# Kernel tuning notes

Hardware: AMD Instinct MI355X
Metric: run time of the kernel (lower is better)

## Reference

```python
import jax, jax.numpy as jnp
import numpy as np

MARGIN = 1.0
EPS = 1e-6  # F.pairwise_distance adds eps to the elementwise diff


def setup_inputs() -> dict:
    key = jax.random.key(0)
    k1, k2, k3 = jax.random.split(key, 3)
    N, D = 8192, 64
    anchor_embeddings = jax.random.normal(k1, (N, D), dtype=jnp.float32)
    positive_embeddings = jax.random.normal(k2, (N, D), dtype=jnp.float32)
    labels = jax.random.randint(k3, (N,), 0, 2, dtype=jnp.int64)
    return {
        "anchor_embeddings": anchor_embeddings,
        "positive_embeddings": positive_embeddings,
        "labels": labels,
    }


def _pairwise_dist(a, p):
    # dist[i, j] = ||(a_i + eps) - p_j||_2, matching F.pairwise_distance's
    # norm(x1 - x2 + eps). Computed via the Gram trick to avoid an [N,N,D]
    # intermediate.
    a = a + EPS
    a2 = jnp.sum(a * a, axis=-1)                      # [N]
    p2 = jnp.sum(p * p, axis=-1)                      # [N]
    sq = a2[:, None] + p2[None, :] - 2.0 * (a @ p.T)  # [N, N]
    return jnp.sqrt(jnp.maximum(sq, 1e-12))


def reference(anchor_embeddings, positive_embeddings, labels):
    N = anchor_embeddings.shape[0]
    dist = _pairwise_dist(anchor_embeddings, positive_embeddings)  # [N, N]
    pos_dist = jnp.diagonal(dist)                                  # [N], d(a_i, p_i)
    hinge = jax.nn.relu(pos_dist[:, None] - dist + MARGIN)         # [N, N]
    # pair (i, j) contributes iff labels[i] == 1 and i != j
    row_mask = (labels == 1)[:, None]
    offdiag = ~jnp.eye(N, dtype=bool)
    mask = (row_mask & offdiag).astype(hinge.dtype)
    count = jnp.sum(mask)
    total = jnp.sum(hinge * mask)
    return jnp.where(count > 0, total / jnp.maximum(count, 1.0), 0.0)
```

## Files before the change

### kernel.cpp

```cpp
#include <hip/hip_runtime.h>
#include <hip/hip_bf16.h>

#define NROWS 8192
#define DDIM 64
#define MARGIN_F 1.0f
#define EPS_F 1e-6f


typedef __attribute__((ext_vector_type(8))) short bf16x8;
typedef __attribute__((ext_vector_type(4))) float f32x4;

static __device__ __forceinline__ unsigned short f2bf(float x) {
    __hip_bfloat16 h = __float2bfloat16(x);
    return *reinterpret_cast<unsigned short*>(&h);
}
static __device__ __forceinline__ float bf2f(unsigned short u) {
    return __uint_as_float(((unsigned)u) << 16);
}

__global__ __launch_bounds__(256) void
prep_compact_kernel(const float* __restrict__ A, const float* __restrict__ P,
                    const int* __restrict__ labels,
                    unsigned short* __restrict__ Abf, unsigned short* __restrict__ Pbf,
                    float* __restrict__ a2g, float* __restrict__ pdg,
                    float* __restrict__ p2g, float* __restrict__ hdg,
                    int* __restrict__ sel, int* __restrict__ cnt) {
    __shared__ int lab[256 * 33];
    __shared__ int scan[256];
    int t = threadIdx.x;

    if (blockIdx.x < 512) {
        int gid = blockIdx.x * 256 + t;
        int row = gid >> 4;
        int c4  = (gid & 15) * 4;
        float4 a = *(const float4*)&A[row * DDIM + c4];
        float4 p = *(const float4*)&P[row * DDIM + c4];
        a.x += EPS_F; a.y += EPS_F; a.z += EPS_F; a.w += EPS_F;
        ushort4 ab, pb;
        ab.x = f2bf(a.x); ab.y = f2bf(a.y); ab.z = f2bf(a.z); ab.w = f2bf(a.w);
        pb.x = f2bf(p.x); pb.y = f2bf(p.y); pb.z = f2bf(p.z); pb.w = f2bf(p.w);
        *(ushort4*)&Abf[row * DDIM + c4] = ab;
        *(ushort4*)&Pbf[row * DDIM + c4] = pb;
        float va2 = a.x*a.x + a.y*a.y + a.z*a.z + a.w*a.w;
        float vp2 = p.x*p.x + p.y*p.y + p.z*p.z + p.w*p.w;
        float vap = a.x*p.x + a.y*p.y + a.z*p.z + a.w*p.w;
        float vdd = bf2f(ab.x)*bf2f(pb.x) + bf2f(ab.y)*bf2f(pb.y)
                  + bf2f(ab.z)*bf2f(pb.z) + bf2f(ab.w)*bf2f(pb.w);
        #pragma unroll
        for (int off = 8; off; off >>= 1) {
            va2 += __shfl_xor(va2, off);
            vp2 += __shfl_xor(vp2, off);
            vap += __shfl_xor(vap, off);
            vdd += __shfl_xor(vdd, off);
        }
        if ((t & 15) == 0) {
            a2g[row] = va2;
            p2g[row] = vp2;
            float pd = sqrtf(fmaxf(va2 + vp2 - 2.0f * vap, 1e-12f)) + MARGIN_F;
            pdg[row] = pd;
            float sqd = fmaxf(va2 + vp2 - 2.0f * vdd, 1e-12f);
            hdg[row] = fmaxf(pd - __builtin_amdgcn_sqrtf(sqd), 0.0f);
        }
    } else {
        #pragma unroll
        for (int i = 0; i < 32; ++i) {
            int j = i * 256 + t;
            lab[(j >> 5) * 33 + (j & 31)] = labels[j];
        }
        __syncthreads();
        int lc = 0;
        #pragma unroll
        for (int i = 0; i < 32; ++i) lc += (lab[t * 33 + i] == 1) ? 1 : 0;
        scan[t] = lc;
        __syncthreads();
        for (int off = 1; off < 256; off <<= 1) {
            int v = (t >= off) ? scan[t - off] : 0;
            __syncthreads();
            if (t >= off) scan[t] += v;
            __syncthreads();
        }
        int o = scan[t] - lc;
        for (int i = 0; i < 32; ++i) {
            if (lab[t * 33 + i] == 1) sel[o++] = t * 32 + i;
        }
        if (t == 255) *cnt = scan[255];
    }
}

__global__ __launch_bounds__(256) void
main_kernel(const unsigned short* __restrict__ Abf, const unsigned short* __restrict__ Pbf,
            const float* __restrict__ a2g, const float* __restrict__ pdg,
            const float* __restrict__ p2g, const int* __restrict__ sel,
            const int* __restrict__ cnt, float* __restrict__ partial) {
    __shared__ float sA2[128], sPd[128], sP2[128];
    __shared__ int   sGi[128];
    __shared__ float wsum[4];

    int M = *cnt;
    int row0 = blockIdx.y << 7;
    int col0 = blockIdx.x << 7;
    int bid  = (blockIdx.y << 6) + blockIdx.x;
    int t = threadIdx.x;
    if (row0 >= M) { if (t == 0) partial[bid] = 0.0f; return; }

    int wid  = t >> 6;
    int lane = t & 63;
    int wm   = (wid >> 1) << 6;
    int wn   = (wid & 1) << 6;
    int lm   = lane & 15;
    int quad = lane >> 4;

    bf16x8 bg[2][4];
    #pragma unroll
    for (int b = 0; b < 4; ++b) {
        const unsigned short* pb = Pbf + (size_t)(col0 + wn + b * 16 + lm) * DDIM + quad * 8;
        bg[0][b] = *(const bf16x8*)pb;
        bg[1][b] = *(const bf16x8*)(pb + 32);
    }

    if (t < 128) {
        int gi = sel[min(row0 + t, M - 1)];
        sGi[t] = gi;
        sA2[t] = a2g[gi];
        sPd[t] = pdg[gi];
        sP2[t] = p2g[col0 + t];
    }
    __syncthreads();

    bf16x8 af[2][4];
    #pragma unroll
    for (int a = 0; a < 4; ++a) {
        const unsigned short* pa = Abf + (size_t)sGi[wm + a * 16 + lm] * DDIM + quad * 8;
        af[0][a] = *(const bf16x8*)pa;
        af[1][a] = *(const bf16x8*)(pa + 32);
    }

    f32x4 acc[4][4] = {};
    #pragma unroll
    for (int s = 0; s < 2; ++s)
        #pragma unroll
        for (int a = 0; a < 4; ++a)
            #pragma unroll
            for (int b = 0; b < 4; ++b)
                acc[a][b] = __builtin_amdgcn_mfma_f32_16x16x32_bf16(af[s][a], bg[s][b], acc[a][b], 0, 0, 0);

    float spv[4];
    #pragma unroll
    for (int b = 0; b < 4; ++b) spv[b] = sP2[wn + b * 16 + lm];

    float bsum = 0.0f;
    #pragma unroll
    for (int a = 0; a < 4; ++a) {
        #pragma unroll
        for (int r = 0; r < 4; ++r) {
            int il = wm + a * 16 + quad * 4 + r;
            float rm  = ((row0 + il) < M) ? 1.0f : 0.0f;
            float ra2 = sA2[il];
            float rpd = sPd[il];
            #pragma unroll
            for (int b = 0; b < 4; ++b) {
                float sq = fmaf(-2.0f, acc[a][b][r], ra2 + spv[b]);
                float h  = rpd - __builtin_amdgcn_sqrtf(sq);
                bsum = fmaf(fmaxf(h, 0.0f), rm, bsum);
            }
        }
    }

    #pragma unroll
    for (int off = 32; off; off >>= 1) bsum += __shfl_xor(bsum, off);
    if (lane == 0) wsum[wid] = bsum;
    __syncthreads();
    if (t == 0) partial[bid] = wsum[0] + wsum[1] + wsum[2] + wsum[3];
}

__global__ __launch_bounds__(256) void
finalize_kernel(const int* __restrict__ cnt, const float* __restrict__ partial,
                const float* __restrict__ hdg, const int* __restrict__ sel,
                float* __restrict__ out) {
    __shared__ float wsum[4];
    int t = threadIdx.x;
    const float4* p4 = (const float4*)partial;
    float s = 0.0f;
    #pragma unroll
    for (int i = 0; i < 4; ++i) {
        float4 v = p4[i * 256 + t];
        s += v.x + v.y + v.z + v.w;
    }
    int M = *cnt;
    for (int idx = t; idx < M; idx += 256) s -= hdg[sel[idx]];
    #pragma unroll
    for (int off = 32; off; off >>= 1) s += __shfl_xor(s, off);
    if ((t & 63) == 0) wsum[t >> 6] = s;
    __syncthreads();
    if (t == 0) {
        float tot = wsum[0] + wsum[1] + wsum[2] + wsum[3];
        float c = (float)M * (float)(NROWS - 1);
        out[0] = (M > 0) ? tot / c : 0.0f;
    }
}

extern "C" void kernel_launch(void* const* d_in, const int* in_sizes, int n_in,
                              void* d_out, int out_size, void* d_ws, size_t ws_size,
                              hipStream_t stream) {
    const float* A      = (const float*)d_in[0];
    const float* P      = (const float*)d_in[1];
    const int*   labels = (const int*)d_in[2];
    float* out = (float*)d_out;

    char* ws = (char*)d_ws;
    unsigned short* Abf = (unsigned short*)(ws);
    unsigned short* Pbf = (unsigned short*)(ws + (1 << 20));
    float* a2g     = (float*)(ws + (2 << 20));
    float* pdg     = (float*)(ws + (2 << 20) + 32768);
    float* p2g     = (float*)(ws + (2 << 20) + 65536);
    int*   sel     = (int*)(ws + (2 << 20) + 98304);
    int*   cnt     = (int*)(ws + (2 << 20) + 131072);
    float* partial = (float*)(ws + (2 << 20) + 135168);
    float* hdg     = (float*)(ws + (2 << 20) + 151552);

    prep_compact_kernel<<<dim3(513), dim3(256), 0, stream>>>(A, P, labels, Abf, Pbf,
                                                             a2g, pdg, p2g, hdg, sel, cnt);

    dim3 grid(NROWS / 128, NROWS / 128);
    main_kernel<<<grid, dim3(256), 0, stream>>>(Abf, Pbf, a2g, pdg, p2g, sel, cnt, partial);

    finalize_kernel<<<1, dim3(256), 0, stream>>>(cnt, partial, hdg, sel, out);
}
```

Measured before the change: 89.96 us.

## Fuse finalize into main kernel via last-block reduction and widen column tiles

Removes the separate finalize launch: each main-kernel block writes its partial sum, bumps an atomic counter, and the last block to finish performs the final reduction and the diagonal correction. Each block now covers four 128-column tiles in a loop, so the grid shrinks from 64x64 to 16x64 and the A fragments and row constants are loaded once per block instead of once per tile. Invalid padded rows are masked by setting their positive distance to a large negative value, which drops the per-element multiply mask. The trade-offs are fewer blocks in flight and an atomic plus threadfence on every block.

```diff
diff --git a/kernel.cpp b/kernel.cpp
--- a/kernel.cpp
+++ b/kernel.cpp
@@ -5,6 +5,7 @@
 #define DDIM 64
 #define MARGIN_F 1.0f
 #define EPS_F 1e-6f
+#define NEG_BIG -1.0e30f
 
 
 typedef __attribute__((ext_vector_type(8))) short bf16x8;
@@ -24,7 +25,8 @@
                     unsigned short* __restrict__ Abf, unsigned short* __restrict__ Pbf,
                     float* __restrict__ a2g, float* __restrict__ pdg,
                     float* __restrict__ p2g, float* __restrict__ hdg,
-                    int* __restrict__ sel, int* __restrict__ cnt) {
+                    int* __restrict__ sel, int* __restrict__ cnt,
+                    unsigned int* __restrict__ done) {
     __shared__ int lab[256 * 33];
     __shared__ int scan[256];
     int t = threadIdx.x;
@@ -62,6 +64,7 @@
             hdg[row] = fmaxf(pd - __builtin_amdgcn_sqrtf(sqd), 0.0f);
         }
     } else {
+        if (t == 0) *done = 0u;
         #pragma unroll
         for (int i = 0; i < 32; ++i) {
             int j = i * 256 + t;
@@ -90,112 +93,125 @@
 __global__ __launch_bounds__(256) void
 main_kernel(const unsigned short* __restrict__ Abf, const unsigned short* __restrict__ Pbf,
             const float* __restrict__ a2g, const float* __restrict__ pdg,
-            const float* __restrict__ p2g, const int* __restrict__ sel,
-            const int* __restrict__ cnt, float* __restrict__ partial) {
-    __shared__ float sA2[128], sPd[128], sP2[128];
+            const float* __restrict__ p2g, const float* __restrict__ hdg,
+            const int* __restrict__ sel, const int* __restrict__ cnt,
+            float* __restrict__ partial, unsigned int* __restrict__ done,
+            float* __restrict__ out) {
+    __shared__ float sA2[128], sPd[128];
     __shared__ int   sGi[128];
     __shared__ float wsum[4];
+    __shared__ int   lastFlag;
 
     int M = *cnt;
+    int t = threadIdx.x;
     int row0 = blockIdx.y << 7;
-    int col0 = blockIdx.x << 7;
-    int bid  = (blockIdx.y << 6) + blockIdx.x;
-    int t = threadIdx.x;
-    if (row0 >= M) { if (t == 0) partial[bid] = 0.0f; return; }
+    int bid  = (blockIdx.y << 4) + blockIdx.x;
 
     int wid  = t >> 6;
     int lane = t & 63;
-    int wm   = (wid >> 1) << 6;
-    int wn   = (wid & 1) << 6;
-    int lm   = lane & 15;
-    int quad = lane >> 4;
-
-    bf16x8 bg[2][4];
-    #pragma unroll
-    for (int b = 0; b < 4; ++b) {
-        const unsigned short* pb = Pbf + (size_t)(col0 + wn + b * 16 + lm) * DDIM + quad * 8;
-        bg[0][b] = *(const bf16x8*)pb;
-        bg[1][b] = *(const bf16x8*)(pb + 32);
-    }
-
-    if (t < 128) {
-        int gi = sel[min(row0 + t, M - 1)];
-        sGi[t] = gi;
-        sA2[t] = a2g[gi];
-        sPd[t] = pdg[gi];
-        sP2[t] = p2g[col0 + t];
+
+    if (row0 < M) {
+        if (t < 128) {
+            int ri = row0 + t;
+            int gi = sel[min(ri, M - 1)];
+            sGi[t] = gi;
+            sA2[t] = a2g[gi];
+            sPd[t] = (ri < M) ? pdg[gi] : NEG_BIG;
+        }
+        __syncthreads();
+
+        int wm   = (wid >> 1) << 6;
+        int wn   = (wid & 1) << 6;
+        int lm   = lane & 15;
+        int quad = lane >> 4;
+
+        bf16x8 af0[4], af1[4];
+        #pragma unroll
+        for (int a = 0; a < 4; ++a) {
+            const unsigned short* pa = Abf + (size_t)sGi[wm + a * 16 + lm] * DDIM + quad * 8;
+            af0[a] = *(const bf16x8*)pa;
+            af1[a] = *(const bf16x8*)(pa + 32);
+        }
+        float ra2s[16], rpds[16];
+        #pragma unroll
+        for (int a = 0; a < 4; ++a)
+            #pragma unroll
+            for (int r = 0; r < 4; ++r) {
+                int il = wm + a * 16 + quad * 4 + r;
+                ra2s[a * 4 + r] = sA2[il];
+                rpds[a * 4 + r] = sPd[il];
+            }
+
+        float bsum = 0.0f;
+        #pragma unroll 1
+        for (int i = 0; i < 4; ++i) {
+            int col0 = (blockIdx.x << 9) + (i << 7);
+            bf16x8 bg0[4], bg1[4];
+            float spv[4];
+            #pragma unroll
+            for (int b = 0; b < 4; ++b) {
+                int cj = col0 + wn + b * 16 + lm;
+                const unsigned short* pb = Pbf + (size_t)cj * DDIM + quad * 8;
+                bg0[b] = *(const bf16x8*)pb;
+                bg1[b] = *(const bf16x8*)(pb + 32);
+                spv[b] = p2g[cj];
+            }
+            f32x4 acc[4][4] = {};
+            #pragma unroll
+            for (int a = 0; a < 4; ++a)
+                #pragma unroll
+                for (int b = 0; b < 4; ++b)
+                    acc[a][b] = __builtin_amdgcn_mfma_f32_16x16x32_bf16(af0[a], bg0[b], acc[a][b], 0, 0, 0);
+            #pragma unroll
+            for (int a = 0; a < 4; ++a)
+                #pragma unroll
+                for (int b = 0; b < 4; ++b)
+                    acc[a][b] = __builtin_amdgcn_mfma_f32_16x16x32_bf16(af1[a], bg1[b], acc[a][b], 0, 0, 0);
+
+            #pragma unroll
+            for (int a = 0; a < 4; ++a)
+                #pragma unroll
+                for (int r = 0; r < 4; ++r) {
+                    float ra2 = ra2s[a * 4 + r];
+                    float rpd = rpds[a * 4 + r];
+                    #pragma unroll
+                    for (int b = 0; b < 4; ++b) {
+                        float sq = fmaf(-2.0f, acc[a][b][r], ra2 + spv[b]);
+                        float h  = rpd - __builtin_amdgcn_sqrtf(sq);
+                        bsum += fmaxf(h, 0.0f);
+                    }
+                }
+        }
+
+        #pragma unroll
+        for (int off = 32; off; off >>= 1) bsum += __shfl_xor(bsum, off);
+        if (lane == 0) wsum[wid] = bsum;
+        __syncthreads();
+    }
+
+    if (t == 0) {
+        float s = (row0 < M) ? (wsum[0] + wsum[1] + wsum[2] + wsum[3]) : 0.0f;
+        partial[bid] = s;
+        __threadfence();
+        unsigned v = atomicAdd(done, 1u);
+        lastFlag = (v == 1023u);
     }
     __syncthreads();
-
-    bf16x8 af[2][4];
-    #pragma unroll
-    for (int a = 0; a < 4; ++a) {
-        const unsigned short* pa = Abf + (size_t)sGi[wm + a * 16 + lm] * DDIM + quad * 8;
-        af[0][a] = *(const bf16x8*)pa;
-        af[1][a] = *(const bf16x8*)(pa + 32);
-    }
-
-    f32x4 acc[4][4] = {};
-    #pragma unroll
-    for (int s = 0; s < 2; ++s)
-        #pragma unroll
-        for (int a = 0; a < 4; ++a)
-            #pragma unroll
-            for (int b = 0; b < 4; ++b)
-                acc[a][b] = __builtin_amdgcn_mfma_f32_16x16x32_bf16(af[s][a], bg[s][b], acc[a][b], 0, 0, 0);
-
-    float spv[4];
-    #pragma unroll
-    for (int b = 0; b < 4; ++b) spv[b] = sP2[wn + b * 16 + lm];
-
-    float bsum = 0.0f;
-    #pragma unroll
-    for (int a = 0; a < 4; ++a) {
-        #pragma unroll
-        for (int r = 0; r < 4; ++r) {
-            int il = wm + a * 16 + quad * 4 + r;
-            float rm  = ((row0 + il) < M) ? 1.0f : 0.0f;
-            float ra2 = sA2[il];
-            float rpd = sPd[il];
-            #pragma unroll
-            for (int b = 0; b < 4; ++b) {
-                float sq = fmaf(-2.0f, acc[a][b][r], ra2 + spv[b]);
-                float h  = rpd - __builtin_amdgcn_sqrtf(sq);
-                bsum = fmaf(fmaxf(h, 0.0f), rm, bsum);
-            }
-        }
-    }
-
-    #pragma unroll
-    for (int off = 32; off; off >>= 1) bsum += __shfl_xor(bsum, off);
-    if (lane == 0) wsum[wid] = bsum;
-    __syncthreads();
-    if (t == 0) partial[bid] = wsum[0] + wsum[1] + wsum[2] + wsum[3];
-}
-
-__global__ __launch_bounds__(256) void
-finalize_kernel(const int* __restrict__ cnt, const float* __restrict__ partial,
-                const float* __restrict__ hdg, const int* __restrict__ sel,
-                float* __restrict__ out) {
-    __shared__ float wsum[4];
-    int t = threadIdx.x;
-    const float4* p4 = (const float4*)partial;
+    if (!lastFlag) return;
+
     float s = 0.0f;
     #pragma unroll
-    for (int i = 0; i < 4; ++i) {
-        float4 v = p4[i * 256 + t];
-        s += v.x + v.y + v.z + v.w;
-    }
-    int M = *cnt;
-    for (int idx = t; idx < M; idx += 256) s -= hdg[sel[idx]];
+    for (int i = 0; i < 4; ++i)
+        s += atomicAdd(&partial[t + i * 256], 0.0f);
+    for (int i = t; i < M; i += 256)
+        s -= hdg[sel[i]];
     #pragma unroll
     for (int off = 32; off; off >>= 1) s += __shfl_xor(s, off);
-    if ((t & 63) == 0) wsum[t >> 6] = s;
+    if ((t & 63) == 0) wsum[wid] = s;
     __syncthreads();
     if (t == 0) {
         float tot = wsum[0] + wsum[1] + wsum[2] + wsum[3];
-        float c = (float)M * (float)(NROWS - 1);
-        out[0] = (M > 0) ? tot / c : 0.0f;
+        out[0] = (M > 0) ? tot / ((float)M * (float)(NROWS - 1)) : 0.0f;
     }
 }
 
@@ -210,19 +226,20 @@
     char* ws = (char*)d_ws;
     unsigned short* Abf = (unsigned short*)(ws);
     unsigned short* Pbf = (unsigned short*)(ws + (1 << 20));
-    float* a2g     = (float*)(ws + (2 << 20));
-    float* pdg     = (float*)(ws + (2 << 20) + 32768);
-    float* p2g     = (float*)(ws + (2 << 20) + 65536);
-    int*   sel     = (int*)(ws + (2 << 20) + 98304);
-    int*   cnt     = (int*)(ws + (2 << 20) + 131072);
-    float* partial = (float*)(ws + (2 << 20) + 135168);
-    float* hdg     = (float*)(ws + (2 << 20) + 151552);
+    char* base = ws + (2 << 20);
+    float* a2g     = (float*)(base);
+    float* pdg     = (float*)(base + 32768);
+    float* p2g     = (float*)(base + 65536);
+    float* hdg     = (float*)(base + 98304);
+    int*   sel     = (int*)(base + 131072);
+    float* partial = (float*)(base + 163840);
+    int*   cnt     = (int*)(base + 167936);
+    unsigned int* done = (unsigned int*)(base + 167940);
 
     prep_compact_kernel<<<dim3(513), dim3(256), 0, stream>>>(A, P, labels, Abf, Pbf,
-                                                             a2g, pdg, p2g, hdg, sel, cnt);
-
-    dim3 grid(NROWS / 128, NROWS / 128);
-    main_kernel<<<grid, dim3(256), 0, stream>>>(Abf, Pbf, a2g, pdg, p2g, sel, cnt, partial);
-
-    finalize_kernel<<<1, dim3(256), 0, stream>>>(cnt, partial, hdg, sel, out);
-}
+                                                             a2g, pdg, p2g, hdg, sel,
+                                                             cnt, done);
+
+    main_kernel<<<dim3(16, 64), dim3(256), 0, stream>>>(Abf, Pbf, a2g, pdg, p2g, hdg,
+                                                        sel, cnt, partial, done, out);
+}
```

Measured after the change: 97.28 us. 1.08x slower.
